# Performance work log

Hardware: AMD Instinct MI355X
Metric: run time of the kernel (lower is better)

Reference implementation:

```python
import jax, jax.numpy as jnp
import numpy as np

N_NODES = 50000
N_EDGES = 800000
D_IN, D_HID, D_OUT = 64, 64, 1


def gcn_layer(x, src, dst, W, b):
    """GCN conv: linear transform, then degree-normalized scatter-add over edges
    (with self-loops), matching x' = D^-1/2 (A+I) D^-1/2 X W^T + b."""
    n = x.shape[0]
    h = x @ W.T + b                                   # [N, out]
    deg = jax.ops.segment_sum(jnp.ones_like(dst, dtype=h.dtype), dst,
                              num_segments=n) + 1.0   # +1 for self-loop
    inv_sqrt_deg = jax.lax.rsqrt(deg)                 # [N]
    coef = inv_sqrt_deg[src] * inv_sqrt_deg[dst]      # [E]
    msgs = h[src] * coef[:, None]                     # gather + scale
    agg = jax.ops.segment_sum(msgs, dst, num_segments=n)   # scatter-add
    agg = agg + h * (inv_sqrt_deg * inv_sqrt_deg)[:, None]  # self-loop term
    return agg


def setup_inputs() -> dict:
    key = jax.random.key(0)
    k = jax.random.split(key, 9)
    x = jax.random.normal(k[0], (N_NODES, D_IN), dtype=jnp.float32)
    edge_index = jax.random.randint(k[1], (2, N_EDGES), 0, N_NODES, dtype=jnp.int64)
    s = 0.1
    W0 = jax.random.normal(k[2], (D_HID, D_IN), dtype=jnp.float32) * s
    b0 = jnp.zeros((D_HID,), dtype=jnp.float32)
    W1 = jax.random.normal(k[3], (D_HID, D_HID), dtype=jnp.float32) * s
    b1 = jnp.zeros((D_HID,), dtype=jnp.float32)
    W2 = jax.random.normal(k[4], (D_OUT, D_HID), dtype=jnp.float32) * s
    b2 = jnp.zeros((D_OUT,), dtype=jnp.float32)
    return {"x": x, "edge_index": edge_index,
            "W0": W0, "b0": b0, "W1": W1, "b1": b1, "W2": W2, "b2": b2}


def reference(x, edge_index, W0, b0, W1, b1, W2, b2):
    src, dst = edge_index[0], edge_index[1]
    h = jax.nn.relu(gcn_layer(x, src, dst, W0, b0))
    h = jax.nn.relu(gcn_layer(h, src, dst, W1, b1))
    out = gcn_layer(h, src, dst, W2, b2)   # [N, 1] per-node logits
    return out
```

## Files before the change

kernel.cpp:

```cpp
#include <hip/hip_runtime.h>

#define N_NODES 50000
#define N_EDGES 800000
#define DMAX 64
#define ZROW N_NODES
#define NB 196
#define CELL 40
#define P1_BLKS 512
#define LIN_BLKS 3125
#define CHFL (50001 * 16)
#define CHF4 (50001 * 4)
#define GSUB 1563
typedef unsigned short u16;
typedef float fv2 __attribute__((ext_vector_type(2)));

__global__ __launch_bounds__(256) void bin_lin0_k(
    const int* __restrict__ src, const int* __restrict__ dst,
    unsigned* __restrict__ payload, unsigned char* __restrict__ counts,
    const float* __restrict__ x, const float* __restrict__ W,
    const float* __restrict__ b, float* __restrict__ hA)
{
    __shared__ float4 smem4[2009];
    int bid = blockIdx.x;
    int tid = threadIdx.x;
    if (bid < P1_BLKS) {
        unsigned* cur = (unsigned*)smem4;
        unsigned* pay = cur + NB;
        for (int i = tid; i < NB; i += 256) cur[i] = 0;
        __syncthreads();
        const int4* dst4 = (const int4*)dst;
        const int4* src4 = (const int4*)src;
        const int NQ = N_EDGES / 4;
        for (int q = bid * 256 + tid; q < NQ; q += P1_BLKS * 256) {
            int4 d = dst4[q];
            int4 s = src4[q];
#define BIN(dd, ss)                                                        \
            {                                                              \
                int bkt = (dd) >> 8;                                       \
                unsigned v = ((unsigned)(ss) << 8) | ((unsigned)(dd) & 255u); \
                int p = atomicAdd((int*)&cur[bkt], 1);                     \
                if (p < CELL) pay[bkt * CELL + p] = v;                     \
            }
            BIN(d.x, s.x) BIN(d.y, s.y) BIN(d.z, s.z) BIN(d.w, s.w)
#undef BIN
        }
        __syncthreads();
        unsigned* pg = payload + (size_t)bid * (NB * CELL);
        for (int i = tid; i < NB * CELL; i += 256) pg[i] = pay[i];
        for (int i = tid; i < NB; i += 256)
            counts[bid * NB + i] = (unsigned char)min((int)cur[i], CELL);
    } else {
        float* Ws = (float*)smem4;
        float* xs = (float*)smem4 + 64 * 68;
        int j = tid & 63, ln = tid >> 6;
        int nb = (bid - P1_BLKS) * 16;
        const float4* W4 = (const float4*)W;
#pragma unroll
        for (int i = 0; i < 4; ++i) {
            int idx4 = i * 256 + tid;
            *(float4*)&Ws[(idx4 >> 4) * 68 + (idx4 & 15) * 4] = W4[idx4];
        }
        {
            const float4* x4 = (const float4*)(x + (size_t)nb * 64);
            float4 v = x4[tid];
            *(float4*)&xs[(tid >> 4) * 68 + (tid & 15) * 4] = v;
        }
        __syncthreads();
        float a0 = b[j], a1 = a0, a2 = a0, a3 = a0;
        const float4* wp = (const float4*)&Ws[j * 68];
        const float4* p0 = (const float4*)&xs[(ln * 4 + 0) * 68];
        const float4* p1 = (const float4*)&xs[(ln * 4 + 1) * 68];
        const float4* p2 = (const float4*)&xs[(ln * 4 + 2) * 68];
        const float4* p3 = (const float4*)&xs[(ln * 4 + 3) * 68];
#pragma unroll
        for (int k4 = 0; k4 < 16; ++k4) {
            float4 w = wp[k4];
            float4 q0 = p0[k4]; a0 += w.x*q0.x + w.y*q0.y + w.z*q0.z + w.w*q0.w;
            float4 q1 = p1[k4]; a1 += w.x*q1.x + w.y*q1.y + w.z*q1.z + w.w*q1.w;
            float4 q2 = p2[k4]; a2 += w.x*q2.x + w.y*q2.y + w.z*q2.z + w.w*q2.w;
            float4 q3 = p3[k4]; a3 += w.x*q3.x + w.y*q3.y + w.z*q3.z + w.w*q3.w;
        }
        size_t cbase = (size_t)(j >> 4) * CHFL + (j & 15);
        hA[cbase + (size_t)(nb + ln * 4 + 0) * 16] = a0;
        hA[cbase + (size_t)(nb + ln * 4 + 1) * 16] = a1;
        hA[cbase + (size_t)(nb + ln * 4 + 2) * 16] = a2;
        hA[cbase + (size_t)(nb + ln * 4 + 3) * 16] = a3;
    }
}

__global__ __launch_bounds__(256) void place_k(
    const unsigned* __restrict__ payload, const unsigned char* __restrict__ counts,
    int* __restrict__ cnt, u16* __restrict__ csr,
    float* __restrict__ hA, float* __restrict__ hB)
{
    __shared__ int cur[256];
    int b = blockIdx.x, tid = threadIdx.x;
    cur[tid] = 0;
    __syncthreads();
    int base = b << 8;
    for (int sb = tid; sb < P1_BLKS; sb += 256) {
        int c = counts[sb * NB + b];
        const unsigned* cell = payload + ((size_t)sb * NB + b) * CELL;
        for (int k = 0; k < c; ++k) {
            unsigned v = cell[k];
            int loc = (int)(v & 255u);
            int slot = atomicAdd(&cur[loc], 1);
            if (slot < DMAX) csr[(size_t)(base + loc) * 64 + slot] = (u16)(v >> 8);
        }
    }
    __syncthreads();
    int n = base + tid;
    if (n < N_NODES) {
        int c = cur[tid];
        cnt[n] = c;
        int m = min(c, DMAX);
        for (int k = m; k < DMAX; ++k) csr[(size_t)n * 64 + k] = (u16)ZROW;
        float inv = rsqrtf((float)c + 1.f);
#pragma unroll
        for (int ch = 0; ch < 4; ++ch) {
            float4* row = (float4*)&hA[(size_t)ch * CHFL + (size_t)n * 16];
#pragma unroll
            for (int i2 = 0; i2 < 4; ++i2) {
                float4 t = row[i2];
                t.x *= inv; t.y *= inv; t.z *= inv; t.w *= inv;
                row[i2] = t;
            }
        }
    }
    if (b == 0 && tid < 64) {
        int ch = tid >> 4, pos = tid & 15;
        hA[(size_t)ch * CHFL + (size_t)ZROW * 16 + pos] = 0.f;
        hB[(size_t)ch * CHFL + (size_t)ZROW * 16 + pos] = 0.f;
        csr[(size_t)ZROW * 64 + tid] = (u16)ZROW;
        if (tid == 0) cnt[ZROW] = 0;
    }
}

__device__ __forceinline__ fv2 chunk_gather(
    const float* __restrict__ hc, const int* __restrict__ cnt,
    const u16* __restrict__ csr, u16* lds_w ,
    int nq, int lane, int oct, int r, float& invn_out, int& nmy_out)
{
#pragma unroll
    for (int i = 0; i < 4; ++i) {
        int u = i * 64 + lane;
        int row = u >> 5, col = u & 31;
        int nn = nq + row;
        nn = nn < N_NODES ? nn : ZROW;
        *(unsigned*)&lds_w[row * 68 + col * 2] = ((const unsigned*)csr)[nn * 32 + col];
    }
    int nmy = nq + oct;
    nmy_out = nmy;
    int nuse = nmy < N_NODES ? nmy : ZROW;
    int mc = cnt[nuse];
    float invn = rsqrtf((float)mc + 1.f);
    invn_out = invn;
    int m8 = (min(mc, DMAX) + 7) & ~7;
    int kmax = m8;
    kmax = max(kmax, __shfl_xor(kmax, 8, 64));
    kmax = max(kmax, __shfl_xor(kmax, 16, 64));
    kmax = max(kmax, __shfl_xor(kmax, 32, 64));
    __builtin_amdgcn_wave_barrier();
    const fv2* h2p = (const fv2*)hc;
    fv2 acc = h2p[(unsigned)(nuse * 8 + r)];
    const u16* myrow = lds_w + oct * 68;
#pragma unroll 1
    for (int k = 0; k < kmax; k += 8) {
#pragma unroll
        for (int u = 0; u < 8; ++u) {
            int s = (int)myrow[k + u];
            fv2 v = h2p[(unsigned)(s * 8 + r)];
            acc.x += v.x; acc.y += v.y;
        }
    }
    return acc;
}

__global__ __launch_bounds__(256) void gath1_k(const float* __restrict__ hA,
                                               const int* __restrict__ cnt,
                                               const u16* __restrict__ csr,
                                               float* __restrict__ rs) {
    __shared__ u16 cs[4][8][68];
    int tid = threadIdx.x, lane = tid & 63, w = tid >> 6;
    int oct = (tid >> 3) & 7, r = tid & 7;
    int set = blockIdx.x & 3, sub = blockIdx.x >> 2;
    int nq = sub * 32 + w * 8;
    const float* hc = hA + (size_t)set * CHFL;
    float invn; int nmy;
    fv2 acc = chunk_gather(hc, cnt, csr, &cs[w][0][0], nq, lane, oct, r, invn, nmy);
    if (nmy < N_NODES) {
        fv2 o;
        o.x = fmaxf(acc.x * invn, 0.f);
        o.y = fmaxf(acc.y * invn, 0.f);
        __builtin_nontemporal_store(o, &((fv2*)(rs + (size_t)set * CHFL))[nmy * 8 + r]);
    }
}

__global__ __launch_bounds__(256) void mv1_k(const float* __restrict__ rs,
                                             const int* __restrict__ cnt,
                                             const float* __restrict__ W,
                                             const float* __restrict__ b,
                                             float* __restrict__ hB) {
    __shared__ float Ws[64 * 68];
    __shared__ float xs[16 * 68];
    int tid = threadIdx.x, j = tid & 63, ln = tid >> 6;
    int nb = blockIdx.x * 16;
    const float4* W4 = (const float4*)W;
#pragma unroll
    for (int i = 0; i < 4; ++i) {
        int idx4 = i * 256 + tid;
        *(float4*)&Ws[(idx4 >> 4) * 68 + (idx4 & 15) * 4] = W4[idx4];
    }
    {
        int t = tid >> 4, r16 = tid & 15, c = r16 >> 2, f4 = r16 & 3;
        int n = nb + t;
        float4 v = ((const float4*)rs)[(size_t)c * CHF4 + (size_t)n * 4 + f4];
        *(float4*)&xs[t * 68 + c * 16 + f4 * 4] = v;
    }
    __syncthreads();
    float a0 = b[j], a1 = a0, a2 = a0, a3 = a0;
    const float4* wp = (const float4*)&Ws[j * 68];
    const float4* p0 = (const float4*)&xs[(ln * 4 + 0) * 68];
    const float4* p1 = (const float4*)&xs[(ln * 4 + 1) * 68];
    const float4* p2 = (const float4*)&xs[(ln * 4 + 2) * 68];
    const float4* p3 = (const float4*)&xs[(ln * 4 + 3) * 68];
#pragma unroll
    for (int k4 = 0; k4 < 16; ++k4) {
        float4 w = wp[k4];
        float4 q0 = p0[k4]; a0 += w.x*q0.x + w.y*q0.y + w.z*q0.z + w.w*q0.w;
        float4 q1 = p1[k4]; a1 += w.x*q1.x + w.y*q1.y + w.z*q1.z + w.w*q1.w;
        float4 q2 = p2[k4]; a2 += w.x*q2.x + w.y*q2.y + w.z*q2.z + w.w*q2.w;
        float4 q3 = p3[k4]; a3 += w.x*q3.x + w.y*q3.y + w.z*q3.z + w.w*q3.w;
    }
    size_t cbase = (size_t)(j >> 4) * CHFL + (j & 15);
    {
        int n0 = nb + ln * 4;
        float i0 = rsqrtf((float)cnt[n0 + 0] + 1.f);
        float i1 = rsqrtf((float)cnt[n0 + 1] + 1.f);
        float i2 = rsqrtf((float)cnt[n0 + 2] + 1.f);
        float i3 = rsqrtf((float)cnt[n0 + 3] + 1.f);
        hB[cbase + (size_t)(n0 + 0) * 16] = a0 * i0;
        hB[cbase + (size_t)(n0 + 1) * 16] = a1 * i1;
        hB[cbase + (size_t)(n0 + 2) * 16] = a2 * i2;
        hB[cbase + (size_t)(n0 + 3) * 16] = a3 * i3;
    }
}

__global__ __launch_bounds__(256) void gath2_k(const float* __restrict__ hB,
                                               const int* __restrict__ cnt,
                                               const u16* __restrict__ csr,
                                               const float* __restrict__ W2,
                                               float* __restrict__ pd) {
    __shared__ u16 cs[4][8][68];
    int tid = threadIdx.x, lane = tid & 63, w = tid >> 6;
    int oct = (tid >> 3) & 7, r = tid & 7;
    int set = blockIdx.x & 3, sub = blockIdx.x >> 2;
    int nq = sub * 32 + w * 8;
    const float* hc = hB + (size_t)set * CHFL;
    float invn; int nmy;
    fv2 acc = chunk_gather(hc, cnt, csr, &cs[w][0][0], nq, lane, oct, r, invn, nmy);
    float f0 = W2[set * 16 + r * 2], f1 = W2[set * 16 + r * 2 + 1];
    float p = fmaxf(acc.x * invn, 0.f) * f0 + fmaxf(acc.y * invn, 0.f) * f1;
    p += __shfl_xor(p, 1, 64);
    p += __shfl_xor(p, 2, 64);
    p += __shfl_xor(p, 4, 64);
    if (r == 0 && nmy < N_NODES) pd[(size_t)set * N_NODES + nmy] = p;
}

__global__ __launch_bounds__(256) void comb_k(const float* __restrict__ pd,
                                              const int* __restrict__ cnt,
                                              const float* __restrict__ b2,
                                              float* __restrict__ h2) {
    int n = blockIdx.x * 256 + threadIdx.x;
    if (n < N_NODES) {
        float s = pd[n] + pd[N_NODES + n] + pd[2 * N_NODES + n] + pd[3 * N_NODES + n];
        h2[n] = (s + b2[0]) * rsqrtf((float)cnt[n] + 1.f);
    }
}

__global__ __launch_bounds__(256) void g1_k(const float* __restrict__ h2,
                                            const int* __restrict__ cnt,
                                            const u16* __restrict__ csr,
                                            float* __restrict__ out) {
    int tid = threadIdx.x, j = tid & 63, w = tid >> 6;
    int nb = blockIdx.x * 16;
#pragma unroll 1
    for (int t = 0; t < 4; ++t) {
        int n = nb + w * 4 + t;
        int mf = cnt[n];
        int m = min(mf, DMAX);
        float invn = rsqrtf((float)mf + 1.f);
        float v = 0.f;
        if (j < m) v = h2[(int)csr[(size_t)n * 64 + j]];
#pragma unroll
        for (int off = 32; off; off >>= 1) v += __shfl_xor(v, off, 64);
        if (j == 0) out[n] = (v + h2[n]) * invn;
    }
}

extern "C" void kernel_launch(void* const* d_in, const int* in_sizes, int n_in,
                              void* d_out, int out_size, void* d_ws, size_t ws_size,
                              hipStream_t stream) {
    const float* x  = (const float*)d_in[0];
    const int*   ei = (const int*)d_in[1];
    const float* W0 = (const float*)d_in[2];
    const float* b0 = (const float*)d_in[3];
    const float* W1 = (const float*)d_in[4];
    const float* b1 = (const float*)d_in[5];
    const float* W2 = (const float*)d_in[6];
    const float* b2 = (const float*)d_in[7];
    float* out = (float*)d_out;

    char* ws = (char*)d_ws;
    size_t off = 0;
    auto alloc = [&](size_t bytes) {
        void* p = ws + off;
        off = (off + bytes + 255) & ~(size_t)255;
        return p;
    };
    int*      cnt  = (int*)alloc((size_t)(N_NODES + 1) * 4);
    u16*      csr  = (u16*)alloc((size_t)(N_NODES + 1) * DMAX * 2);
    float*    hA   = (float*)alloc((size_t)4 * CHFL * 4);
    float*    hB   = (float*)alloc((size_t)4 * CHFL * 4);
    float*    rs   = (float*)alloc((size_t)4 * CHFL * 4);
    float*    pd   = (float*)alloc((size_t)4 * N_NODES * 4);
    float*    h2   = (float*)alloc((size_t)N_NODES * 4);
    unsigned* payload = (unsigned*)alloc((size_t)P1_BLKS * NB * CELL * 4);
    unsigned char* counts = (unsigned char*)alloc((size_t)P1_BLKS * NB);

    const int* src = ei;
    const int* dst = ei + N_EDGES;

    bin_lin0_k<<<P1_BLKS + LIN_BLKS, 256, 0, stream>>>(src, dst, payload, counts,
                                                       x, W0, b0, hA);
    place_k<<<NB, 256, 0, stream>>>(payload, counts, cnt, csr, hA, hB);
    gath1_k<<<GSUB * 4, 256, 0, stream>>>(hA, cnt, csr, rs);
    mv1_k<<<LIN_BLKS, 256, 0, stream>>>(rs, cnt, W1, b1, hB);
    gath2_k<<<GSUB * 4, 256, 0, stream>>>(hB, cnt, csr, W2, pd);
    comb_k<<<196, 256, 0, stream>>>(pd, cnt, b2, h2);
    g1_k<<<LIN_BLKS, 256, 0, stream>>>(h2, cnt, csr, out);
}
```

Measured before the change: 118.2 us.

## Store hidden feature buffers in bf16 with 32-wide channel chunks

Converts the intermediate node-feature buffers (hA, hB, rs) from fp32 to bf16, with round-to-nearest-even packing and unpacking to fp32 for accumulation. The channel split changes from four 16-float chunks to two 32-bf16 chunks, so each gather thread still loads 8 bytes but now covers 4 features, which halves the gather grids and the partial-dot buffer. The goal is to halve the memory traffic of the bandwidth-bound edge gathers and the linear layers, at the cost of bf16 rounding error in the hidden activations.

Result: faster. 94.74 us (median of 3 runs) (-19.8%).

```diff
diff --git a/kernel.cpp b/kernel.cpp
--- a/kernel.cpp
+++ b/kernel.cpp
@@ -8,17 +8,27 @@
 #define CELL 40
 #define P1_BLKS 512
 #define LIN_BLKS 3125
-#define CHFL (50001 * 16)
-#define CHF4 (50001 * 4)
+#define CH (50001 * 32)
 #define GSUB 1563
 typedef unsigned short u16;
-typedef float fv2 __attribute__((ext_vector_type(2)));
+
+__device__ __forceinline__ u16 f2bf(float f) {
+    unsigned u = __builtin_bit_cast(unsigned, f);
+    u += 0x7FFFu + ((u >> 16) & 1u);
+    return (u16)(u >> 16);
+}
+__device__ __forceinline__ float bflo(unsigned u) {
+    return __builtin_bit_cast(float, u << 16);
+}
+__device__ __forceinline__ float bfhi(unsigned u) {
+    return __builtin_bit_cast(float, u & 0xFFFF0000u);
+}
 
 __global__ __launch_bounds__(256) void bin_lin0_k(
     const int* __restrict__ src, const int* __restrict__ dst,
     unsigned* __restrict__ payload, unsigned char* __restrict__ counts,
     const float* __restrict__ x, const float* __restrict__ W,
-    const float* __restrict__ b, float* __restrict__ hA)
+    const float* __restrict__ b, u16* __restrict__ hA)
 {
     __shared__ float4 smem4[2009];
     int bid = blockIdx.x;
@@ -80,18 +90,18 @@
             float4 q2 = p2[k4]; a2 += w.x*q2.x + w.y*q2.y + w.z*q2.z + w.w*q2.w;
             float4 q3 = p3[k4]; a3 += w.x*q3.x + w.y*q3.y + w.z*q3.z + w.w*q3.w;
         }
-        size_t cbase = (size_t)(j >> 4) * CHFL + (j & 15);
-        hA[cbase + (size_t)(nb + ln * 4 + 0) * 16] = a0;
-        hA[cbase + (size_t)(nb + ln * 4 + 1) * 16] = a1;
-        hA[cbase + (size_t)(nb + ln * 4 + 2) * 16] = a2;
-        hA[cbase + (size_t)(nb + ln * 4 + 3) * 16] = a3;
+        size_t cbase = (size_t)(j >> 5) * CH + (j & 31);
+        hA[cbase + (size_t)(nb + ln * 4 + 0) * 32] = f2bf(a0);
+        hA[cbase + (size_t)(nb + ln * 4 + 1) * 32] = f2bf(a1);
+        hA[cbase + (size_t)(nb + ln * 4 + 2) * 32] = f2bf(a2);
+        hA[cbase + (size_t)(nb + ln * 4 + 3) * 32] = f2bf(a3);
     }
 }
 
 __global__ __launch_bounds__(256) void place_k(
     const unsigned* __restrict__ payload, const unsigned char* __restrict__ counts,
     int* __restrict__ cnt, u16* __restrict__ csr,
-    float* __restrict__ hA, float* __restrict__ hB)
+    u16* __restrict__ hA, u16* __restrict__ hB)
 {
     __shared__ int cur[256];
     int b = blockIdx.x, tid = threadIdx.x;
@@ -117,27 +127,27 @@
         for (int k = m; k < DMAX; ++k) csr[(size_t)n * 64 + k] = (u16)ZROW;
         float inv = rsqrtf((float)c + 1.f);
 #pragma unroll
-        for (int ch = 0; ch < 4; ++ch) {
-            float4* row = (float4*)&hA[(size_t)ch * CHFL + (size_t)n * 16];
-#pragma unroll
-            for (int i2 = 0; i2 < 4; ++i2) {
-                float4 t = row[i2];
-                t.x *= inv; t.y *= inv; t.z *= inv; t.w *= inv;
-                row[i2] = t;
+        for (int ch = 0; ch < 2; ++ch) {
+            unsigned* row = (unsigned*)&hA[(size_t)ch * CH + (size_t)n * 32];
+#pragma unroll
+            for (int i2 = 0; i2 < 16; ++i2) {
+                unsigned u = row[i2];
+                float lo = bflo(u) * inv, hi = bfhi(u) * inv;
+                row[i2] = ((unsigned)f2bf(hi) << 16) | f2bf(lo);
             }
         }
     }
     if (b == 0 && tid < 64) {
-        int ch = tid >> 4, pos = tid & 15;
-        hA[(size_t)ch * CHFL + (size_t)ZROW * 16 + pos] = 0.f;
-        hB[(size_t)ch * CHFL + (size_t)ZROW * 16 + pos] = 0.f;
+        int ch = tid >> 5, pos = tid & 31;
+        hA[(size_t)ch * CH + (size_t)ZROW * 32 + pos] = 0;
+        hB[(size_t)ch * CH + (size_t)ZROW * 32 + pos] = 0;
         csr[(size_t)ZROW * 64 + tid] = (u16)ZROW;
         if (tid == 0) cnt[ZROW] = 0;
     }
 }
 
-__device__ __forceinline__ fv2 chunk_gather(
-    const float* __restrict__ hc, const int* __restrict__ cnt,
+__device__ __forceinline__ float4 cgather(
+    const u16* __restrict__ hc, const int* __restrict__ cnt,
     const u16* __restrict__ csr, u16* lds_w ,
     int nq, int lane, int oct, int r, float& invn_out, int& nmy_out)
 {
@@ -161,46 +171,51 @@
     kmax = max(kmax, __shfl_xor(kmax, 16, 64));
     kmax = max(kmax, __shfl_xor(kmax, 32, 64));
     __builtin_amdgcn_wave_barrier();
-    const fv2* h2p = (const fv2*)hc;
-    fv2 acc = h2p[(unsigned)(nuse * 8 + r)];
+    const uint2* hp = (const uint2*)hc;
+    uint2 sv = hp[(unsigned)(nuse * 8 + r)];
+    float a0 = bflo(sv.x), a1 = bfhi(sv.x), a2 = bflo(sv.y), a3 = bfhi(sv.y);
     const u16* myrow = lds_w + oct * 68;
 #pragma unroll 1
     for (int k = 0; k < kmax; k += 8) {
 #pragma unroll
         for (int u = 0; u < 8; ++u) {
             int s = (int)myrow[k + u];
-            fv2 v = h2p[(unsigned)(s * 8 + r)];
-            acc.x += v.x; acc.y += v.y;
-        }
-    }
-    return acc;
-}
-
-__global__ __launch_bounds__(256) void gath1_k(const float* __restrict__ hA,
+            uint2 v = hp[(unsigned)(s * 8 + r)];
+            a0 += bflo(v.x); a1 += bfhi(v.x);
+            a2 += bflo(v.y); a3 += bfhi(v.y);
+        }
+    }
+    float4 o; o.x = a0; o.y = a1; o.z = a2; o.w = a3;
+    return o;
+}
+
+__global__ __launch_bounds__(256) void gath1_k(const u16* __restrict__ hA,
                                                const int* __restrict__ cnt,
                                                const u16* __restrict__ csr,
-                                               float* __restrict__ rs) {
+                                               u16* __restrict__ rs) {
     __shared__ u16 cs[4][8][68];
     int tid = threadIdx.x, lane = tid & 63, w = tid >> 6;
     int oct = (tid >> 3) & 7, r = tid & 7;
-    int set = blockIdx.x & 3, sub = blockIdx.x >> 2;
+    int set = blockIdx.x & 1, sub = blockIdx.x >> 1;
     int nq = sub * 32 + w * 8;
-    const float* hc = hA + (size_t)set * CHFL;
+    const u16* hc = hA + (size_t)set * CH;
     float invn; int nmy;
-    fv2 acc = chunk_gather(hc, cnt, csr, &cs[w][0][0], nq, lane, oct, r, invn, nmy);
+    float4 a = cgather(hc, cnt, csr, &cs[w][0][0], nq, lane, oct, r, invn, nmy);
     if (nmy < N_NODES) {
-        fv2 o;
-        o.x = fmaxf(acc.x * invn, 0.f);
-        o.y = fmaxf(acc.y * invn, 0.f);
-        __builtin_nontemporal_store(o, &((fv2*)(rs + (size_t)set * CHFL))[nmy * 8 + r]);
-    }
-}
-
-__global__ __launch_bounds__(256) void mv1_k(const float* __restrict__ rs,
+        float f0 = fmaxf(a.x * invn, 0.f), f1 = fmaxf(a.y * invn, 0.f);
+        float f2 = fmaxf(a.z * invn, 0.f), f3 = fmaxf(a.w * invn, 0.f);
+        uint2 o;
+        o.x = ((unsigned)f2bf(f1) << 16) | f2bf(f0);
+        o.y = ((unsigned)f2bf(f3) << 16) | f2bf(f2);
+        ((uint2*)(rs + (size_t)set * CH))[(unsigned)(nmy * 8 + r)] = o;
+    }
+}
+
+__global__ __launch_bounds__(256) void mv1_k(const u16* __restrict__ rs,
                                              const int* __restrict__ cnt,
                                              const float* __restrict__ W,
                                              const float* __restrict__ b,
-                                             float* __restrict__ hB) {
+                                             u16* __restrict__ hB) {
     __shared__ float Ws[64 * 68];
     __shared__ float xs[16 * 68];
     int tid = threadIdx.x, j = tid & 63, ln = tid >> 6;
@@ -212,10 +227,13 @@
         *(float4*)&Ws[(idx4 >> 4) * 68 + (idx4 & 15) * 4] = W4[idx4];
     }
     {
-        int t = tid >> 4, r16 = tid & 15, c = r16 >> 2, f4 = r16 & 3;
+        int t = tid >> 4, r16 = tid & 15;
+        int c = r16 >> 3, g = r16 & 7;
         int n = nb + t;
-        float4 v = ((const float4*)rs)[(size_t)c * CHF4 + (size_t)n * 4 + f4];
-        *(float4*)&xs[t * 68 + c * 16 + f4 * 4] = v;
+        uint2 u = ((const uint2*)(rs + (size_t)c * CH))[(unsigned)(n * 8 + g)];
+        float* xp = &xs[t * 68 + c * 32 + g * 4];
+        xp[0] = bflo(u.x); xp[1] = bfhi(u.x);
+        xp[2] = bflo(u.y); xp[3] = bfhi(u.y);
     }
     __syncthreads();
     float a0 = b[j], a1 = a0, a2 = a0, a3 = a0;
@@ -232,21 +250,19 @@
         float4 q2 = p2[k4]; a2 += w.x*q2.x + w.y*q2.y + w.z*q2.z + w.w*q2.w;
         float4 q3 = p3[k4]; a3 += w.x*q3.x + w.y*q3.y + w.z*q3.z + w.w*q3.w;
     }
-    size_t cbase = (size_t)(j >> 4) * CHFL + (j & 15);
-    {
-        int n0 = nb + ln * 4;
-        float i0 = rsqrtf((float)cnt[n0 + 0] + 1.f);
-        float i1 = rsqrtf((float)cnt[n0 + 1] + 1.f);
-        float i2 = rsqrtf((float)cnt[n0 + 2] + 1.f);
-        float i3 = rsqrtf((float)cnt[n0 + 3] + 1.f);
-        hB[cbase + (size_t)(n0 + 0) * 16] = a0 * i0;
-        hB[cbase + (size_t)(n0 + 1) * 16] = a1 * i1;
-        hB[cbase + (size_t)(n0 + 2) * 16] = a2 * i2;
-        hB[cbase + (size_t)(n0 + 3) * 16] = a3 * i3;
-    }
-}
-
-__global__ __launch_bounds__(256) void gath2_k(const float* __restrict__ hB,
+    size_t cbase = (size_t)(j >> 5) * CH + (j & 31);
+    int n0 = nb + ln * 4;
+    float i0 = rsqrtf((float)cnt[n0 + 0] + 1.f);
+    float i1 = rsqrtf((float)cnt[n0 + 1] + 1.f);
+    float i2 = rsqrtf((float)cnt[n0 + 2] + 1.f);
+    float i3 = rsqrtf((float)cnt[n0 + 3] + 1.f);
+    hB[cbase + (size_t)(n0 + 0) * 32] = f2bf(a0 * i0);
+    hB[cbase + (size_t)(n0 + 1) * 32] = f2bf(a1 * i1);
+    hB[cbase + (size_t)(n0 + 2) * 32] = f2bf(a2 * i2);
+    hB[cbase + (size_t)(n0 + 3) * 32] = f2bf(a3 * i3);
+}
+
+__global__ __launch_bounds__(256) void gath2_k(const u16* __restrict__ hB,
                                                const int* __restrict__ cnt,
                                                const u16* __restrict__ csr,
                                                const float* __restrict__ W2,
@@ -254,13 +270,14 @@
     __shared__ u16 cs[4][8][68];
     int tid = threadIdx.x, lane = tid & 63, w = tid >> 6;
     int oct = (tid >> 3) & 7, r = tid & 7;
-    int set = blockIdx.x & 3, sub = blockIdx.x >> 2;
+    int set = blockIdx.x & 1, sub = blockIdx.x >> 1;
     int nq = sub * 32 + w * 8;
-    const float* hc = hB + (size_t)set * CHFL;
+    const u16* hc = hB + (size_t)set * CH;
     float invn; int nmy;
-    fv2 acc = chunk_gather(hc, cnt, csr, &cs[w][0][0], nq, lane, oct, r, invn, nmy);
-    float f0 = W2[set * 16 + r * 2], f1 = W2[set * 16 + r * 2 + 1];
-    float p = fmaxf(acc.x * invn, 0.f) * f0 + fmaxf(acc.y * invn, 0.f) * f1;
+    float4 a = cgather(hc, cnt, csr, &cs[w][0][0], nq, lane, oct, r, invn, nmy);
+    const float4 wv = ((const float4*)W2)[set * 8 + r];
+    float p = fmaxf(a.x * invn, 0.f) * wv.x + fmaxf(a.y * invn, 0.f) * wv.y
+            + fmaxf(a.z * invn, 0.f) * wv.z + fmaxf(a.w * invn, 0.f) * wv.w;
     p += __shfl_xor(p, 1, 64);
     p += __shfl_xor(p, 2, 64);
     p += __shfl_xor(p, 4, 64);
@@ -273,7 +290,7 @@
                                               float* __restrict__ h2) {
     int n = blockIdx.x * 256 + threadIdx.x;
     if (n < N_NODES) {
-        float s = pd[n] + pd[N_NODES + n] + pd[2 * N_NODES + n] + pd[3 * N_NODES + n];
+        float s = pd[n] + pd[N_NODES + n];
         h2[n] = (s + b2[0]) * rsqrtf((float)cnt[n] + 1.f);
     }
 }
@@ -320,10 +337,10 @@
     };
     int*      cnt  = (int*)alloc((size_t)(N_NODES + 1) * 4);
     u16*      csr  = (u16*)alloc((size_t)(N_NODES + 1) * DMAX * 2);
-    float*    hA   = (float*)alloc((size_t)4 * CHFL * 4);
-    float*    hB   = (float*)alloc((size_t)4 * CHFL * 4);
-    float*    rs   = (float*)alloc((size_t)4 * CHFL * 4);
-    float*    pd   = (float*)alloc((size_t)4 * N_NODES * 4);
+    u16*      hA   = (u16*)alloc((size_t)2 * CH * 2);
+    u16*      hB   = (u16*)alloc((size_t)2 * CH * 2);
+    u16*      rs   = (u16*)alloc((size_t)2 * CH * 2);
+    float*    pd   = (float*)alloc((size_t)2 * N_NODES * 4);
     float*    h2   = (float*)alloc((size_t)N_NODES * 4);
     unsigned* payload = (unsigned*)alloc((size_t)P1_BLKS * NB * CELL * 4);
     unsigned char* counts = (unsigned char*)alloc((size_t)P1_BLKS * NB);
@@ -334,9 +351,9 @@
     bin_lin0_k<<<P1_BLKS + LIN_BLKS, 256, 0, stream>>>(src, dst, payload, counts,
                                                        x, W0, b0, hA);
     place_k<<<NB, 256, 0, stream>>>(payload, counts, cnt, csr, hA, hB);
-    gath1_k<<<GSUB * 4, 256, 0, stream>>>(hA, cnt, csr, rs);
+    gath1_k<<<GSUB * 2, 256, 0, stream>>>(hA, cnt, csr, rs);
     mv1_k<<<LIN_BLKS, 256, 0, stream>>>(rs, cnt, W1, b1, hB);
-    gath2_k<<<GSUB * 4, 256, 0, stream>>>(hB, cnt, csr, W2, pd);
+    gath2_k<<<GSUB * 2, 256, 0, stream>>>(hB, cnt, csr, W2, pd);
     comb_k<<<196, 256, 0, stream>>>(pd, cnt, b2, h2);
     g1_k<<<LIN_BLKS, 256, 0, stream>>>(h2, cnt, csr, out);
 }
```
